# Performance work log

Measured on AMD Instinct MI355X. Metric: run time of the kernel, lower is better.

Reference implementation:

```python
import jax, jax.numpy as jnp
import numpy as np

B, N, D, H = 2, 384, 128, 8

def _ln(x, g, b, eps=1e-5):
    m = jnp.mean(x, -1, keepdims=True)
    v = jnp.mean((x - m) ** 2, -1, keepdims=True)
    return (x - m) * jax.lax.rsqrt(v + eps) * g + b

def _gelu(x):
    return jax.nn.gelu(x, approximate=False)  # torch nn.GELU default = exact erf

def setup_inputs() -> dict:
    key = jax.random.key(0)
    ks = jax.random.split(key, 20)
    def w(i, *s):
        return jax.random.normal(ks[i], s, jnp.float32) * 0.02
    return {
        'node_features': jax.random.normal(ks[0], (B, N, D), jnp.float32),
        'edge_features': jax.random.normal(ks[1], (B, N, N, D), jnp.float32),
        'mask': jnp.ones((B, N), dtype=bool),
        'attn_wqkv_node': w(2, D, 3 * D),
        'attn_wqkv_edge': w(3, D, 4 * D),
        'lin0_w': w(4, D, D), 'lin0_b': jnp.zeros(D, jnp.float32),
        'ln0_g': jnp.ones(D, jnp.float32), 'ln0_bias': jnp.zeros(D, jnp.float32),
        'ln1_g': jnp.ones(D, jnp.float32), 'ln1_bias': jnp.zeros(D, jnp.float32),
        'nmlp_w1': w(5, D, 2 * D), 'nmlp_w2': w(6, 2 * D, D), 'nmlp_b2': jnp.zeros(D, jnp.float32),
        'e0_we': w(7, 2 * D, D), 'e0_be': jnp.zeros(D, jnp.float32),
        'e0_ws': w(8, D, D), 'e0_bs': jnp.zeros(D, jnp.float32),
        'e0_wt': w(9, D, D), 'e0_bt': jnp.zeros(D, jnp.float32),
        'e0_wer': w(10, D, D), 'e0_wec': w(11, D, D),
        'e0_w1': w(12, D, D), 'e0_b1': jnp.zeros(D, jnp.float32),
        'e1_w1': w(13, D, 2 * D), 'e1_w2': w(14, 2 * D, D), 'e1_b2': jnp.zeros(D, jnp.float32),
        'eln0_g': jnp.ones(D, jnp.float32), 'eln0_b': jnp.zeros(D, jnp.float32),
        'eln1_g': jnp.ones(D, jnp.float32), 'eln1_b': jnp.zeros(D, jnp.float32),
    }

def _forward(node, edge, wqkv_n, wqkv_e, lin0_w, lin0_b, ln0_g, ln0_bias, ln1_g, ln1_bias,
             nmlp_w1, nmlp_w2, nmlp_b2, e0_we, e0_be, e0_ws, e0_bs, e0_wt, e0_bt,
             e0_wer, e0_wec, e0_w1, e0_b1, e1_w1, e1_w2, e1_b2, eln0_g, eln0_b, eln1_g, eln1_b):
    b, n, d = node.shape
    h = H
    dh = d // h
    scale = 1.0 / (d ** 0.5)  # note: scale uses full d_hid as in source
    # ---- RTAttention (modulate_v=True) ----
    qkv_n = (node @ wqkv_n).reshape(b, n, h, 3 * dh).transpose(0, 2, 1, 3)  # b h n 3dh
    qn, kn, vn = jnp.split(qkv_n, 3, axis=-1)
    qkv_e = (edge @ wqkv_e).reshape(b, n, n, h, 4 * dh).transpose(0, 3, 1, 2, 4)  # b h i j 4dh
    eq, ek, ev, em = jnp.split(qkv_e, 4, axis=-1)
    q = qn[:, :, :, None, :] + eq                      # b h i j dh
    k = kn[:, :, None, :, :] + ek
    v = vn[:, :, None, :, :] * em + ev                 # modulate_v: v_node*edge[3] + edge[2]
    dots = scale * jnp.einsum('bhijd,bhijd->bhij', q, k)
    attn = jax.nn.softmax(dots, axis=-1)
    out = jnp.einsum('bhij,bhijd->bhid', attn, v)
    out = out.transpose(0, 2, 1, 3).reshape(b, n, d)
    # ---- node updates, type 'rt' (dropout=0 -> identity) ----
    x = _ln(node + (out @ lin0_w + lin0_b), ln0_g, ln0_bias)
    x = _ln(x + (_gelu(x @ nmlp_w1) @ nmlp_w2 + nmlp_b2), ln1_g, ln1_bias)
    # ---- edge updates: EdgeMLP ----
    sn = (x @ e0_ws + e0_bs)[:, :, None, :]                       # broadcast over j
    tn = (x @ e0_wt + e0_bt)[:, None, :, :]                       # broadcast over i
    se = jnp.mean(edge, axis=1, keepdims=True) @ e0_wec           # mean over dim -3, lin0_ec
    te = jnp.mean(edge, axis=2, keepdims=True) @ e0_wer           # mean over dim -2, lin0_er
    e = jnp.concatenate([edge, jnp.swapaxes(edge, 1, 2)], axis=-1) @ e0_we + e0_be
    e = _gelu(e + sn + tn + se + te) @ e0_w1 + e0_b1
    edge2 = _ln(edge + e, eln0_g, eln0_b)
    edge2 = _ln(edge2 + (_gelu(edge2 @ e1_w1) @ e1_w2 + e1_b2), eln1_g, eln1_b)
    return x, edge2

def reference(node_features, edge_features, mask, attn_wqkv_node, attn_wqkv_edge,
              lin0_w, lin0_b, ln0_g, ln0_bias, ln1_g, ln1_bias,
              nmlp_w1, nmlp_w2, nmlp_b2, e0_we, e0_be, e0_ws, e0_bs, e0_wt, e0_bt,
              e0_wer, e0_wec, e0_w1, e0_b1, e1_w1, e1_w2, e1_b2,
              eln0_g, eln0_b, eln1_g, eln1_b):
    # mask is accepted but unused by the source forward path
    return _forward(node_features, edge_features, attn_wqkv_node, attn_wqkv_edge,
                    lin0_w, lin0_b, ln0_g, ln0_bias, ln1_g, ln1_bias,
                    nmlp_w1, nmlp_w2, nmlp_b2, e0_we, e0_be, e0_ws, e0_bs, e0_wt, e0_bt,
                    e0_wer, e0_wec, e0_w1, e0_b1, e1_w1, e1_w2, e1_b2,
                    eln0_g, eln0_b, eln1_g, eln1_b)
```

## Files before the change

### kernel.cpp

```cpp
#include <hip/hip_runtime.h>
#include <hip/hip_bf16.h>
#include <cstdint>
#include <cstddef>

#define B_ 2
#define N_ 384
#define D_ 128
#define NN (N_*N_)
#define BN (B_*N_)
#define EDGE_ELEMS (B_*NN*D_)
#define NODE_ELEMS (BN*D_)

typedef short bh8 __attribute__((ext_vector_type(8)));
typedef float f32x4 __attribute__((ext_vector_type(4)));

__device__ __forceinline__ f32x4 mfma_bf16(bh8 a, bh8 b, f32x4 c){
  return __builtin_amdgcn_mfma_f32_16x16x32_bf16(a, b, c, 0, 0, 0);
}
__device__ __forceinline__ unsigned short f2bf(float f){
  unsigned u = __float_as_uint(f);
  return (unsigned short)((u + 0x7fffu + ((u >> 16) & 1u)) >> 16);
}
__device__ __forceinline__ unsigned f2bf_pk(float a, float b){
  __hip_bfloat162 h = __float22bfloat162_rn(make_float2(a, b));
  return *(unsigned*)&h;
}
__device__ __forceinline__ float bf2f(unsigned short h){
  return __uint_as_float(((unsigned)h) << 16);
}
__device__ __forceinline__ float geluf(float x){
  return 0.5f * x * (1.0f + erff(x * 0.70710678118654752f));
}
__device__ __forceinline__ float gelu_fast(float x){
  float x2 = x * x;
  float t  = __fmaf_rn(0.044715f * x, x2, x);
  float e  = __expf(1.5957691216057308f * t);
  float r  = __builtin_amdgcn_rcpf(e + 1.0f);
  return x - x * r;
}
__device__ __forceinline__ f32x4 zero4(){ f32x4 z = {0.f,0.f,0.f,0.f}; return z; }

__device__ __forceinline__ float red16_add(float x){
  x += __int_as_float(__builtin_amdgcn_update_dpp(0, __float_as_int(x), 0xB1, 0xF, 0xF, true));
  x += __int_as_float(__builtin_amdgcn_update_dpp(0, __float_as_int(x), 0x4E, 0xF, 0xF, true));
  x += __int_as_float(__builtin_amdgcn_update_dpp(0, __float_as_int(x), 0x141, 0xF, 0xF, true));
  x += __int_as_float(__builtin_amdgcn_update_dpp(0, __float_as_int(x), 0x140, 0xF, 0xF, true));
  return x;
}
__device__ __forceinline__ float red4_add(float x){
  x += __int_as_float(__builtin_amdgcn_update_dpp(0, __float_as_int(x), 0xB1, 0xF, 0xF, true));
  x += __int_as_float(__builtin_amdgcn_update_dpp(0, __float_as_int(x), 0x4E, 0xF, 0xF, true));
  return x;
}
__device__ __forceinline__ int swz(int m, int c){
  return ((((c >> 3) ^ (m & 7)) << 3) | (c & 7));
}

__global__ void kprep(const float* wqkv_e, const float* e0_we, const float* e0_w1,
                      const float* e1_w1, const float* e1_w2,
                      const float* node, const float* wqkv_n,
                      unsigned short* WqkvT, unsigned short* WeT, unsigned short* W1T,
                      unsigned short* E1W1T, unsigned short* E1W2T,
                      float* qkvn){
  int m = blockIdx.y;
  int tid = threadIdx.x;
  if (m < 5){
    const float* src; unsigned short* dst; int K, Nn;
    if (m == 0){ src = wqkv_e; dst = WqkvT; K = 128; Nn = 512; }
    else if (m == 1){ src = e0_we; dst = WeT;   K = 256; Nn = 128; }
    else if (m == 2){ src = e0_w1; dst = W1T;   K = 128; Nn = 128; }
    else if (m == 3){ src = e1_w1; dst = E1W1T; K = 128; Nn = 256; }
    else            { src = e1_w2; dst = E1W2T; K = 256; Nn = 128; }
    int idx = blockIdx.x * 384 + tid;
    if (idx < K * Nn){
      int n = idx / K, k = idx % K;
      dst[idx] = f2bf(src[k * Nn + n]);
    }
  } else {
    int row = blockIdx.x;
    __shared__ float sn[128];
    if (tid < 128) sn[tid] = node[row * 128 + tid];
    __syncthreads();
    float acc = 0.f;
    #pragma unroll 8
    for (int k = 0; k < 128; ++k) acc += sn[k] * wqkv_n[k * 384 + tid];
    qkvn[row * 384 + tid] = acc;
  }
}

__global__ void kprepA(const float* __restrict__ edge, unsigned short* __restrict__ E16,
                       float* __restrict__ meanJ){
  __shared__ float red[8][128];
  int bi = blockIdx.x; int tid = threadIdx.x;
  const float4* src = (const float4*)(edge + (size_t)bi * N_ * D_);
  uint2* gdst = (uint2*)E16 + (size_t)bi * (N_ * D_ / 4);
  float ps0 = 0.f, ps1 = 0.f, ps2 = 0.f, ps3 = 0.f;
  #pragma unroll 4
  for (int k = 0; k < 48; ++k){
    int idx = k * 256 + tid;
    float4 v = src[idx];
    uint2 o;
    o.x = f2bf_pk(v.x, v.y);
    o.y = f2bf_pk(v.z, v.w);
    gdst[idx] = o;
    ps0 += v.x; ps1 += v.y; ps2 += v.z; ps3 += v.w;
  }
  int g = tid >> 5, d0 = (tid & 31) * 4;
  red[g][d0] = ps0; red[g][d0 + 1] = ps1; red[g][d0 + 2] = ps2; red[g][d0 + 3] = ps3;
  __syncthreads();
  if (tid < 128){
    float s = 0.f;
    #pragma unroll
    for (int gg = 0; gg < 8; ++gg) s += red[gg][tid];
    meanJ[bi * 128 + tid] = s * (1.0f / N_);
  }
}

__global__ __launch_bounds__(256, 2) void kattnI(
    const unsigned short* __restrict__ E16, const unsigned short* __restrict__ WqkvT,
    const float* __restrict__ qkvn, float* __restrict__ attn,
    float* __restrict__ meanI){
  __shared__ float red[16][128];
  int tid = threadIdx.x;
  if (blockIdx.y == 1){
    int bj = blockIdx.x; int b = bj / N_, j = bj % N_;
    int ig = tid >> 4, dsub = tid & 15;
    float acc[8];
    #pragma unroll
    for (int e = 0; e < 8; ++e) acc[e] = 0.f;
    #pragma unroll 4
    for (int i = ig; i < N_; i += 16){
      const unsigned short* p = E16 + ((size_t)(b * N_ + i) * N_ + j) * D_ + dsub * 8;
      uint4 u = *(const uint4*)p;
      acc[0] += bf2f((unsigned short)(u.x & 0xffff)); acc[1] += bf2f((unsigned short)(u.x >> 16));
      acc[2] += bf2f((unsigned short)(u.y & 0xffff)); acc[3] += bf2f((unsigned short)(u.y >> 16));
      acc[4] += bf2f((unsigned short)(u.z & 0xffff)); acc[5] += bf2f((unsigned short)(u.z >> 16));
      acc[6] += bf2f((unsigned short)(u.w & 0xffff)); acc[7] += bf2f((unsigned short)(u.w >> 16));
    }
    #pragma unroll
    for (int e = 0; e < 8; ++e) red[ig][dsub * 8 + e] = acc[e];
    __syncthreads();
    if (tid < 128){
      float s = 0.f;
      #pragma unroll
      for (int gg = 0; gg < 16; ++gg) s += red[gg][tid];
      meanI[bj * 128 + tid] = s * (1.0f / N_);
    }
    return;
  }
  int bi = blockIdx.x; int b = bi / N_;
  int w = tid >> 6, lane = tid & 63, quad = lane >> 4, c16 = lane & 15;
  const float scale = 0.08838834764831845f;
  const unsigned short* Abase = E16 + (size_t)bi * N_ * D_;

  bh8 bf[2][4][4];
  #pragma unroll
  for (int s = 0; s < 2; ++s){
    int h = w + s * 4;
    #pragma unroll
    for (int u = 0; u < 4; ++u)
      #pragma unroll
      for (int ks = 0; ks < 4; ++ks){
        int col = h * 64 + u * 16 + c16;
        bf[s][u][ks] = *(const bh8*)(WqkvT + col * 128 + ks * 32 + quad * 8);
      }
  }
  float qv[2];
  #pragma unroll
  for (int s = 0; s < 2; ++s) qv[s] = qkvn[bi * 384 + (w + s * 4) * 48 + c16];

  float m_run[2] = {-1e30f, -1e30f}, l_run[2] = {0.f, 0.f}, o[2] = {0.f, 0.f};
  bh8 af[4];
  #pragma unroll
  for (int ks = 0; ks < 4; ++ks)
    af[ks] = *(const bh8*)(Abase + (size_t)c16 * D_ + ks * 32 + quad * 8);

  for (int jt = 0; jt < 24; ++jt){
    int jn = (jt + 1 < 24) ? jt + 1 : 0;
    bh8 afn[4];
    #pragma unroll
    for (int ks = 0; ks < 4; ++ks)
      afn[ks] = *(const bh8*)(Abase + (size_t)(jn * 16 + c16) * D_ + ks * 32 + quad * 8);
    float knv[2][4], vnv[2][4];
    const float* kvb = qkvn + ((size_t)b * N_ + jt * 16 + quad * 4) * 384;
    #pragma unroll
    for (int s = 0; s < 2; ++s)
      #pragma unroll
      for (int r = 0; r < 4; ++r){
        knv[s][r] = kvb[r * 384 + (w + s * 4) * 48 + 16 + c16];
        vnv[s][r] = kvb[r * 384 + (w + s * 4) * 48 + 32 + c16];
      }
    f32x4 EQ[2], EK[2], EV[2], EM[2];
    #pragma unroll
    for (int s = 0; s < 2; ++s){ EQ[s] = zero4(); EK[s] = zero4(); EV[s] = zero4(); EM[s] = zero4(); }
    #pragma unroll
    for (int ks = 0; ks < 4; ++ks)
      #pragma unroll
      for (int s = 0; s < 2; ++s){
        EQ[s] = mfma_bf16(af[ks], bf[s][0][ks], EQ[s]);
        EK[s] = mfma_bf16(af[ks], bf[s][1][ks], EK[s]);
        EV[s] = mfma_bf16(af[ks], bf[s][2][ks], EV[s]);
        EM[s] = mfma_bf16(af[ks], bf[s][3][ks], EM[s]);
      }
    #pragma unroll
    for (int s = 0; s < 2; ++s){
      float dots[4], vv[4];
      #pragma unroll
      for (int r = 0; r < 4; ++r){
        float t1 = (qv[s] + EQ[s][r]) * (knv[s][r] + EK[s][r]);
        dots[r] = red16_add(t1) * scale;
        vv[r] = vnv[s][r] * EM[s][r] + EV[s][r];
      }
      float tmax = fmaxf(fmaxf(dots[0], dots[1]), fmaxf(dots[2], dots[3]));
      tmax = fmaxf(tmax, __shfl_xor(tmax, 16));
      tmax = fmaxf(tmax, __shfl_xor(tmax, 32));
      float mnew = fmaxf(m_run[s], tmax);
      float al = __expf(m_run[s] - mnew);
      float p0 = __expf(dots[0] - mnew), p1 = __expf(dots[1] - mnew);
      float p2 = __expf(dots[2] - mnew), p3 = __expf(dots[3] - mnew);
      float lt = p0 + p1 + p2 + p3;
      lt += __shfl_xor(lt, 16); lt += __shfl_xor(lt, 32);
      l_run[s] = l_run[s] * al + lt;
      m_run[s] = mnew;
      o[s] = o[s] * al + p0 * vv[0] + p1 * vv[1] + p2 * vv[2] + p3 * vv[3];
    }
    #pragma unroll
    for (int ks = 0; ks < 4; ++ks) af[ks] = afn[ks];
  }
  #pragma unroll
  for (int s = 0; s < 2; ++s){
    float oo = o[s];
    oo += __shfl_xor(oo, 16); oo += __shfl_xor(oo, 32);
    oo /= l_run[s];
    if (quad == 0) attn[(size_t)bi * D_ + (w + s * 4) * 16 + c16] = oo;
  }
}

__global__ void knodeadd(const float* __restrict__ node, const float* __restrict__ attn,
                         const float* lin0_w, const float* lin0_b,
                         const float* g0, const float* bb0,
                         const float* w1, const float* w2, const float* b2,
                         const float* g1, const float* bb1,
                         const float* __restrict__ meanJ, const float* __restrict__ meanI,
                         const float* ws, const float* bs, const float* wt, const float* bt,
                         const float* wer, const float* wec, const float* be,
                         float* __restrict__ xOut,
                         float* __restrict__ rowAdd, float* __restrict__ colAdd){
  int row = blockIdx.x; int tid = threadIdx.x;
  __shared__ float sa[128], sx[128], sh[256], rb[8], sx2[128], smJ[128], smI[128];
  if (tid < 128){
    sa[tid] = attn[row * 128 + tid];
    smJ[tid] = meanJ[row * 128 + tid];
    smI[tid] = meanI[row * 128 + tid];
  }
  __syncthreads();
  float y = 0.f, x0 = 0.f;
  if (tid < 128){
    float acc = lin0_b[tid];
    #pragma unroll 8
    for (int k = 0; k < 128; ++k) acc += sa[k] * lin0_w[k * 128 + tid];
    y = acc + node[row * 128 + tid];
  }
  { float sv = (tid < 128) ? y : 0.f, sq = (tid < 128) ? y * y : 0.f;
    sv = red16_add(sv); sq = red16_add(sq);
    sv += __shfl_xor(sv, 16); sq += __shfl_xor(sq, 16);
    sv += __shfl_xor(sv, 32); sq += __shfl_xor(sq, 32);
    if ((tid & 63) == 0){ rb[tid >> 6] = sv; rb[4 + (tid >> 6)] = sq; } }
  __syncthreads();
  float mean = (rb[0] + rb[1] + rb[2] + rb[3]) * (1.f / 128.f);
  float var  = (rb[4] + rb[5] + rb[6] + rb[7]) * (1.f / 128.f) - mean * mean;
  float rstd = rsqrtf(var + 1e-5f);
  if (tid < 128){ x0 = (y - mean) * rstd * g0[tid] + bb0[tid]; sx[tid] = x0; }
  __syncthreads();
  { float acc = 0.f;
    #pragma unroll 8
    for (int k = 0; k < 128; ++k) acc += sx[k] * w1[k * 256 + tid];
    sh[tid] = geluf(acc); }
  __syncthreads();
  float y2 = 0.f;
  if (tid < 128){
    float acc = b2[tid];
    #pragma unroll 8
    for (int e = 0; e < 256; ++e) acc += sh[e] * w2[e * 128 + tid];
    y2 = acc + x0;
  }
  __syncthreads();
  { float sv = (tid < 128) ? y2 : 0.f, sq = (tid < 128) ? y2 * y2 : 0.f;
    sv = red16_add(sv); sq = red16_add(sq);
    sv += __shfl_xor(sv, 16); sq += __shfl_xor(sq, 16);
    sv += __shfl_xor(sv, 32); sq += __shfl_xor(sq, 32);
    if ((tid & 63) == 0){ rb[tid >> 6] = sv; rb[4 + (tid >> 6)] = sq; } }
  __syncthreads();
  mean = (rb[0] + rb[1] + rb[2] + rb[3]) * (1.f / 128.f);
  var  = (rb[4] + rb[5] + rb[6] + rb[7]) * (1.f / 128.f) - mean * mean;
  rstd = rsqrtf(var + 1e-5f);
  if (tid < 128){
    float xv = (y2 - mean) * rstd * g1[tid] + bb1[tid];
    xOut[row * 128 + tid] = xv;
    sx2[tid] = xv;
  }
  __syncthreads();
  if (tid < 128){
    int d = tid;
    float s1 = bs[d], s3 = 0.f;
    #pragma unroll 8
    for (int k = 0; k < 128; ++k){
      s1 += sx2[k] * ws[k * 128 + d];
      s3 += smJ[k] * wer[k * 128 + d];
    }
    rowAdd[row * 128 + d] = s1 + s3 + be[d];
  } else {
    int d = tid - 128;
    float s2 = bt[d], s4 = 0.f;
    #pragma unroll 8
    for (int k = 0; k < 128; ++k){
      s2 += sx2[k] * wt[k * 128 + d];
      s4 += smI[k] * wec[k * 128 + d];
    }
    colAdd[row * 128 + d] = s2 + s4;
  }
}

__global__ __launch_bounds__(256, 3) void kedge4(
    const unsigned short* __restrict__ E16, const unsigned short* __restrict__ WeT,
    const unsigned short* __restrict__ W1T, const unsigned short* __restrict__ E1W1T,
    const unsigned short* __restrict__ E1W2T,
    const float* __restrict__ rowAdd, const float* __restrict__ colAdd,
    const float* __restrict__ b1, const float* __restrict__ eg0, const float* __restrict__ eb0,
    const float* __restrict__ e1b2, const float* __restrict__ eg1, const float* __restrict__ eb1,
    float* __restrict__ eOut){
  __shared__ unsigned short sA[64][256];
  __shared__ unsigned short sT[64][128];
  __shared__ float lrS[4][64], lrQ[4][64];
  __shared__ float2 stats[64];
  int tid = threadIdx.x;
  int w = tid >> 6, lane = tid & 63, quad = lane >> 4, c16 = lane & 15;
  int R0 = blockIdx.x * 64;
  int b = R0 / NN; int rem = R0 % NN; int i = rem / N_; int j0 = rem % N_;

  bh8 wb1[2][8];
  #pragma unroll
  for (int t = 0; t < 2; ++t)
    #pragma unroll
    for (int ks = 0; ks < 8; ++ks){
      int col = w * 32 + t * 16 + c16;
      wb1[t][ks] = *(const bh8*)(WeT + (size_t)col * 256 + ks * 32 + quad * 8);
    }
  float ca[2][16], rAv[2];
  #pragma unroll
  for (int t = 0; t < 2; ++t){
    rAv[t] = rowAdd[(b * N_ + i) * D_ + w * 32 + t * 16 + c16];
    #pragma unroll
    for (int ms = 0; ms < 4; ++ms)
      #pragma unroll
      for (int r = 0; r < 4; ++r)
        ca[t][ms * 4 + r] = colAdd[(size_t)(b * N_ + j0 + ms * 16 + quad * 4 + r) * D_
                                   + w * 32 + t * 16 + c16];
  }

  #pragma unroll
  for (int it = 0; it < 8; ++it){
    int cid = it * 256 + tid;
    int rrow = cid >> 5;
    int chunk = cid & 31;
    int kc = chunk * 8;
    const unsigned short* sp;
    if (kc < 128) sp = E16 + ((size_t)(b * N_ + i) * N_ + (j0 + rrow)) * D_ + kc;
    else          sp = E16 + ((size_t)(b * N_ + j0 + rrow) * N_ + i) * D_ + (kc - 128);
    *(float4*)&sA[rrow][(chunk ^ (rrow & 7)) << 3] = *(const float4*)sp;
  }
  __syncthreads();

  f32x4 acc1[2][4];
  #pragma unroll
  for (int t = 0; t < 2; ++t) for (int ms = 0; ms < 4; ++ms) acc1[t][ms] = zero4();
  #pragma unroll
  for (int ks = 0; ks < 8; ++ks){
    bh8 af[4];
    #pragma unroll
    for (int ms = 0; ms < 4; ++ms)
      af[ms] = *(const bh8*)&sA[ms * 16 + c16][((ks * 4 + quad) ^ (c16 & 7)) << 3];
    #pragma unroll
    for (int t = 0; t < 2; ++t)
      #pragma unroll
      for (int ms = 0; ms < 4; ++ms)
        acc1[t][ms] = mfma_bf16(af[ms], wb1[t][ks], acc1[t][ms]);
  }
  #pragma unroll
  for (int ms = 0; ms < 4; ++ms)
    #pragma unroll
    for (int r = 0; r < 4; ++r){
      int m = ms * 16 + quad * 4 + r;
      float v0 = gelu_fast(acc1[0][ms][r] + rAv[0] + ca[0][ms * 4 + r]);
      float v1 = gelu_fast(acc1[1][ms][r] + rAv[1] + ca[1][ms * 4 + r]);
      unsigned pk = f2bf_pk(v0, v1);
      sT[m][swz(m, w * 32 + c16)]      = (unsigned short)(pk & 0xffff);
      sT[m][swz(m, w * 32 + 16 + c16)] = (unsigned short)(pk >> 16);
    }
  __syncthreads();

  bh8 wb2[2][4];
  #pragma unroll
  for (int t = 0; t < 2; ++t)
    #pragma unroll
    for (int ks = 0; ks < 4; ++ks){
      int col = w * 32 + t * 16 + c16;
      wb2[t][ks] = *(const bh8*)(W1T + (size_t)col * 128 + ks * 32 + quad * 8);
    }
  f32x4 acc2[2][4];
  #pragma unroll
  for (int t = 0; t < 2; ++t) for (int ms = 0; ms < 4; ++ms) acc2[t][ms] = zero4();
  #pragma unroll
  for (int ks = 0; ks < 4; ++ks){
    bh8 af[4];
    #pragma unroll
    for (int ms = 0; ms < 4; ++ms)
      af[ms] = *(const bh8*)&sT[ms * 16 + c16][((ks * 4 + quad) ^ (c16 & 7)) << 3];
    #pragma unroll
    for (int t = 0; t < 2; ++t)
      #pragma unroll
      for (int ms = 0; ms < 4; ++ms)
        acc2[t][ms] = mfma_bf16(af[ms], wb2[t][ks], acc2[t][ms]);
  }
  float b1v[2], g0v[2], b0v[2];
  #pragma unroll
  for (int t = 0; t < 2; ++t){
    int c = w * 32 + t * 16 + c16;
    b1v[t] = b1[c]; g0v[t] = eg0[c]; b0v[t] = eb0[c];
  }
  #pragma unroll
  for (int ms = 0; ms < 4; ++ms)
    #pragma unroll
    for (int r = 0; r < 4; ++r){
      int m = ms * 16 + quad * 4 + r;
      float s = 0.f, q = 0.f;
      #pragma unroll
      for (int t = 0; t < 2; ++t){
        float v = acc2[t][ms][r] + b1v[t] + bf2f(sA[m][swz(m, w * 32 + t * 16 + c16)]);
        acc2[t][ms][r] = v; s += v; q += v * v;
      }
      s = red16_add(s); q = red16_add(q);
      if (c16 == 0){ lrS[w][m] = s; lrQ[w][m] = q; }
    }
  __syncthreads();
  {
    int src = lane & 3, mrow = w * 16 + (lane >> 2);
    float sp = lrS[src][mrow], qp = lrQ[src][mrow];
    sp = red4_add(sp); qp = red4_add(qp);
    if (src == 0){
      float mean = sp * (1.f / 128.f);
      float var  = qp * (1.f / 128.f) - mean * mean;
      stats[mrow] = make_float2(mean, rsqrtf(var + 1e-5f));
    }
  }
  __syncthreads();
  #pragma unroll
  for (int ms = 0; ms < 4; ++ms)
    #pragma unroll
    for (int r = 0; r < 4; ++r){
      int m = ms * 16 + quad * 4 + r;
      float2 st = stats[m];
      float e0 = (acc2[0][ms][r] - st.x) * st.y * g0v[0] + b0v[0];
      float e1 = (acc2[1][ms][r] - st.x) * st.y * g0v[1] + b0v[1];
      unsigned pk = f2bf_pk(e0, e1);
      sA[m][swz(m, w * 32 + c16)]      = (unsigned short)(pk & 0xffff);
      sA[m][swz(m, w * 32 + 16 + c16)] = (unsigned short)(pk >> 16);
    }
  __syncthreads();

  f32x4 acc4[2][4];
  #pragma unroll
  for (int t = 0; t < 2; ++t) for (int ms = 0; ms < 4; ++ms) acc4[t][ms] = zero4();
  #pragma unroll
  for (int p = 0; p < 2; ++p){
    bh8 wb3[2][4];
    #pragma unroll
    for (int t = 0; t < 2; ++t)
      #pragma unroll
      for (int ks = 0; ks < 4; ++ks){
        int col = p * 128 + w * 32 + t * 16 + c16;
        wb3[t][ks] = *(const bh8*)(E1W1T + (size_t)col * 128 + ks * 32 + quad * 8);
      }
    f32x4 acc3[2][4];
    #pragma unroll
    for (int t = 0; t < 2; ++t) for (int ms = 0; ms < 4; ++ms) acc3[t][ms] = zero4();
    #pragma unroll
    for (int ks = 0; ks < 4; ++ks){
      bh8 af[4];
      #pragma unroll
      for (int ms = 0; ms < 4; ++ms)
        af[ms] = *(const bh8*)&sA[ms * 16 + c16][((ks * 4 + quad) ^ (c16 & 7)) << 3];
      #pragma unroll
      for (int t = 0; t < 2; ++t)
        #pragma unroll
        for (int ms = 0; ms < 4; ++ms)
          acc3[t][ms] = mfma_bf16(af[ms], wb3[t][ks], acc3[t][ms]);
    }
    #pragma unroll
    for (int ms = 0; ms < 4; ++ms)
      #pragma unroll
      for (int r = 0; r < 4; ++r){
        int m = ms * 16 + quad * 4 + r;
        float v0 = gelu_fast(acc3[0][ms][r]);
        float v1 = gelu_fast(acc3[1][ms][r]);
        unsigned pk = f2bf_pk(v0, v1);
        sT[m][swz(m, w * 32 + c16)]      = (unsigned short)(pk & 0xffff);
        sT[m][swz(m, w * 32 + 16 + c16)] = (unsigned short)(pk >> 16);
      }
    __syncthreads();
    bh8 wb4[2][4];
    #pragma unroll
    for (int t = 0; t < 2; ++t)
      #pragma unroll
      for (int k2 = 0; k2 < 4; ++k2){
        int col = w * 32 + t * 16 + c16;
        wb4[t][k2] = *(const bh8*)(E1W2T + (size_t)col * 256 + p * 128 + k2 * 32 + quad * 8);
      }
    #pragma unroll
    for (int k2 = 0; k2 < 4; ++k2){
      bh8 af[4];
      #pragma unroll
      for (int ms = 0; ms < 4; ++ms)
        af[ms] = *(const bh8*)&sT[ms * 16 + c16][((k2 * 4 + quad) ^ (c16 & 7)) << 3];
      #pragma unroll
      for (int t = 0; t < 2; ++t)
        #pragma unroll
        for (int ms = 0; ms < 4; ++ms)
          acc4[t][ms] = mfma_bf16(af[ms], wb4[t][k2], acc4[t][ms]);
    }
    __syncthreads();
  }

  float b2v[2], g1v[2], bb1v[2];
  #pragma unroll
  for (int t = 0; t < 2; ++t){
    int c = w * 32 + t * 16 + c16;
    b2v[t] = e1b2[c]; g1v[t] = eg1[c]; bb1v[t] = eb1[c];
  }
  #pragma unroll
  for (int ms = 0; ms < 4; ++ms)
    #pragma unroll
    for (int r = 0; r < 4; ++r){
      int m = ms * 16 + quad * 4 + r;
      float s = 0.f, q = 0.f;
      #pragma unroll
      for (int t = 0; t < 2; ++t){
        float v = acc4[t][ms][r] + b2v[t] + bf2f(sA[m][swz(m, w * 32 + t * 16 + c16)]);
        acc4[t][ms][r] = v; s += v; q += v * v;
      }
      s = red16_add(s); q = red16_add(q);
      if (c16 == 0){ lrS[w][m] = s; lrQ[w][m] = q; }
    }
  __syncthreads();
  {
    int src = lane & 3, mrow = w * 16 + (lane >> 2);
    float sp = lrS[src][mrow], qp = lrQ[src][mrow];
    sp = red4_add(sp); qp = red4_add(qp);
    if (src == 0){
      float mean = sp * (1.f / 128.f);
      float var  = qp * (1.f / 128.f) - mean * mean;
      stats[mrow] = make_float2(mean, rsqrtf(var + 1e-5f));
    }
  }
  __syncthreads();
  float* outBase = eOut + ((size_t)(b * N_ + i) * N_ + j0) * D_;
  #pragma unroll
  for (int ms = 0; ms < 4; ++ms)
    #pragma unroll
    for (int r = 0; r < 4; ++r){
      int m = ms * 16 + quad * 4 + r;
      float2 st = stats[m];
      #pragma unroll
      for (int t = 0; t < 2; ++t){
        int c = w * 32 + t * 16 + c16;
        outBase[(size_t)m * D_ + c] = (acc4[t][ms][r] - st.x) * st.y * g1v[t] + bb1v[t];
      }
    }
}

extern "C" void kernel_launch(void* const* d_in, const int* in_sizes, int n_in,
                              void* d_out, int out_size, void* d_ws, size_t ws_size,
                              hipStream_t stream){
  const float* node   = (const float*)d_in[0];
  const float* edge   = (const float*)d_in[1];
  const float* wqkv_n = (const float*)d_in[3];
  const float* wqkv_e = (const float*)d_in[4];
  const float* lin0_w = (const float*)d_in[5];
  const float* lin0_b = (const float*)d_in[6];
  const float* ln0_g  = (const float*)d_in[7];
  const float* ln0_b  = (const float*)d_in[8];
  const float* ln1_g  = (const float*)d_in[9];
  const float* ln1_b  = (const float*)d_in[10];
  const float* nmlp_w1= (const float*)d_in[11];
  const float* nmlp_w2= (const float*)d_in[12];
  const float* nmlp_b2= (const float*)d_in[13];
  const float* e0_we  = (const float*)d_in[14];
  const float* e0_be  = (const float*)d_in[15];
  const float* e0_ws  = (const float*)d_in[16];
  const float* e0_bs  = (const float*)d_in[17];
  const float* e0_wt  = (const float*)d_in[18];
  const float* e0_bt  = (const float*)d_in[19];
  const float* e0_wer = (const float*)d_in[20];
  const float* e0_wec = (const float*)d_in[21];
  const float* e0_w1  = (const float*)d_in[22];
  const float* e0_b1  = (const float*)d_in[23];
  const float* e1_w1  = (const float*)d_in[24];
  const float* e1_w2  = (const float*)d_in[25];
  const float* e1_b2  = (const float*)d_in[26];
  const float* eln0_g = (const float*)d_in[27];
  const float* eln0_b = (const float*)d_in[28];
  const float* eln1_g = (const float*)d_in[29];
  const float* eln1_b = (const float*)d_in[30];

  unsigned short* E16   = (unsigned short*)d_ws;
  unsigned short* WqkvT = E16 + (size_t)EDGE_ELEMS;
  unsigned short* WeT   = WqkvT + 65536;
  unsigned short* W1T   = WeT + 32768;
  unsigned short* E1W1T = W1T + 16384;
  unsigned short* E1W2T = E1W1T + 32768;
  float* fbase  = (float*)(E1W2T + 32768);
  float* qkvn   = fbase;
  float* attn   = qkvn + (size_t)BN * 384;
  float* meanJ  = attn + NODE_ELEMS;
  float* meanI  = meanJ + NODE_ELEMS;
  float* rowAdd = meanI + NODE_ELEMS;
  float* colAdd = rowAdd + NODE_ELEMS;

  float* xOut = (float*)d_out;
  float* eOut = xOut + NODE_ELEMS;

  kprep<<<dim3(BN, 6), 384, 0, stream>>>(wqkv_e, e0_we, e0_w1, e1_w1, e1_w2,
                                         node, wqkv_n,
                                         WqkvT, WeT, W1T, E1W1T, E1W2T, qkvn);
  kprepA<<<BN, 256, 0, stream>>>(edge, E16, meanJ);
  kattnI<<<dim3(BN, 2), 256, 0, stream>>>(E16, WqkvT, qkvn, attn, meanI);
  knodeadd<<<BN, 256, 0, stream>>>(node, attn, lin0_w, lin0_b, ln0_g, ln0_b,
                                   nmlp_w1, nmlp_w2, nmlp_b2, ln1_g, ln1_b,
                                   meanJ, meanI, e0_ws, e0_bs, e0_wt, e0_bt,
                                   e0_wer, e0_wec, e0_be,
                                   xOut, rowAdd, colAdd);
  kedge4<<<NN * B_ / 64, 256, 0, stream>>>(E16, WeT, W1T, E1W1T, E1W2T,
                                           rowAdd, colAdd, e0_b1,
                                           eln0_g, eln0_b, e1_b2, eln1_g, eln1_b,
                                           eOut);
}
```

Baseline: 636.0 us.

## Reuse sA for intermediates, permute weight K order, raise kedge4 occupancy

Removes the separate sT, reduction and stats shared buffers in kedge4 and stores GELU intermediates and LayerNorm partials in the upper half of sA. The K dimension of the W1/E1W1/E1W2 weights is permuted at prep time, so each lane writes adjacent output columns as one packed 32-bit LDS store and one float2 global store. Launch bounds go from 3 to 5 blocks per CU to use the freed LDS. The rowAdd/colAdd loads move after the first GEMM to shorten register live ranges. The cost is extra barriers and a possible risk of register spills under the tighter bound.

```diff
diff --git a/kernel.cpp b/kernel.cpp
--- a/kernel.cpp
+++ b/kernel.cpp
@@ -52,8 +52,11 @@
   x += __int_as_float(__builtin_amdgcn_update_dpp(0, __float_as_int(x), 0x4E, 0xF, 0xF, true));
   return x;
 }
-__device__ __forceinline__ int swz(int m, int c){
-  return ((((c >> 3) ^ (m & 7)) << 3) | (c & 7));
+__device__ __forceinline__ int swz(int m, int p){
+  return ((((p >> 3) ^ (m & 7)) << 3) | (p & 7));
+}
+__device__ __forceinline__ int PHIDX(int x){
+  return (x & ~31) | ((x & 1) << 4) | ((x & 31) >> 1);
 }
 
 __global__ void kprep(const float* wqkv_e, const float* e0_we, const float* e0_w1,
@@ -74,7 +77,8 @@
     int idx = blockIdx.x * 384 + tid;
     if (idx < K * Nn){
       int n = idx / K, k = idx % K;
-      dst[idx] = f2bf(src[k * Nn + n]);
+      int ksrc = (m >= 2) ? ((k & ~127) | PHIDX(k & 127)) : k;
+      dst[idx] = f2bf(src[ksrc * Nn + n]);
     }
   } else {
     int row = blockIdx.x;
@@ -321,7 +325,7 @@
   }
 }
 
-__global__ __launch_bounds__(256, 3) void kedge4(
+__global__ __launch_bounds__(256, 5) void kedge4(
     const unsigned short* __restrict__ E16, const unsigned short* __restrict__ WeT,
     const unsigned short* __restrict__ W1T, const unsigned short* __restrict__ E1W1T,
     const unsigned short* __restrict__ E1W2T,
@@ -330,9 +334,7 @@
     const float* __restrict__ e1b2, const float* __restrict__ eg1, const float* __restrict__ eb1,
     float* __restrict__ eOut){
   __shared__ unsigned short sA[64][256];
-  __shared__ unsigned short sT[64][128];
-  __shared__ float lrS[4][64], lrQ[4][64];
-  __shared__ float2 stats[64];
+#define HIFV(i) (((float*)&sA[0][0])[ (((i) >> 6) << 7) + 64 + ((i) & 63) ])
   int tid = threadIdx.x;
   int w = tid >> 6, lane = tid & 63, quad = lane >> 4, c16 = lane & 15;
   int R0 = blockIdx.x * 64;
@@ -346,17 +348,6 @@
       int col = w * 32 + t * 16 + c16;
       wb1[t][ks] = *(const bh8*)(WeT + (size_t)col * 256 + ks * 32 + quad * 8);
     }
-  float ca[2][16], rAv[2];
-  #pragma unroll
-  for (int t = 0; t < 2; ++t){
-    rAv[t] = rowAdd[(b * N_ + i) * D_ + w * 32 + t * 16 + c16];
-    #pragma unroll
-    for (int ms = 0; ms < 4; ++ms)
-      #pragma unroll
-      for (int r = 0; r < 4; ++r)
-        ca[t][ms * 4 + r] = colAdd[(size_t)(b * N_ + j0 + ms * 16 + quad * 4 + r) * D_
-                                   + w * 32 + t * 16 + c16];
-  }
 
   #pragma unroll
   for (int it = 0; it < 8; ++it){
@@ -378,14 +369,29 @@
   for (int ks = 0; ks < 8; ++ks){
     bh8 af[4];
     #pragma unroll
-    for (int ms = 0; ms < 4; ++ms)
-      af[ms] = *(const bh8*)&sA[ms * 16 + c16][((ks * 4 + quad) ^ (c16 & 7)) << 3];
+    for (int ms = 0; ms < 4; ++ms){
+      int row = ms * 16 + c16;
+      af[ms] = *(const bh8*)&sA[row][swz(row, ks * 32 + quad * 8)];
+    }
     #pragma unroll
     for (int t = 0; t < 2; ++t)
       #pragma unroll
       for (int ms = 0; ms < 4; ++ms)
         acc1[t][ms] = mfma_bf16(af[ms], wb1[t][ks], acc1[t][ms]);
   }
+  float rAv[2], ca[2][16];
+  #pragma unroll
+  for (int t = 0; t < 2; ++t){
+    rAv[t] = rowAdd[(b * N_ + i) * D_ + w * 32 + t * 16 + c16];
+    #pragma unroll
+    for (int ms = 0; ms < 4; ++ms)
+      #pragma unroll
+      for (int r = 0; r < 4; ++r)
+        ca[t][ms * 4 + r] = colAdd[(size_t)(b * N_ + j0 + ms * 16 + quad * 4 + r) * D_
+                                   + w * 32 + t * 16 + c16];
+  }
+  __syncthreads();
+
   #pragma unroll
   for (int ms = 0; ms < 4; ++ms)
     #pragma unroll
@@ -393,9 +399,7 @@
       int m = ms * 16 + quad * 4 + r;
       float v0 = gelu_fast(acc1[0][ms][r] + rAv[0] + ca[0][ms * 4 + r]);
       float v1 = gelu_fast(acc1[1][ms][r] + rAv[1] + ca[1][ms * 4 + r]);
-      unsigned pk = f2bf_pk(v0, v1);
-      sT[m][swz(m, w * 32 + c16)]      = (unsigned short)(pk & 0xffff);
-      sT[m][swz(m, w * 32 + 16 + c16)] = (unsigned short)(pk >> 16);
+      *(unsigned*)&sA[m][swz(m, 128 + w * 32 + c16 * 2)] = f2bf_pk(v0, v1);
     }
   __syncthreads();
 
@@ -414,8 +418,10 @@
   for (int ks = 0; ks < 4; ++ks){
     bh8 af[4];
     #pragma unroll
-    for (int ms = 0; ms < 4; ++ms)
-      af[ms] = *(const bh8*)&sT[ms * 16 + c16][((ks * 4 + quad) ^ (c16 & 7)) << 3];
+    for (int ms = 0; ms < 4; ++ms){
+      int row = ms * 16 + c16;
+      af[ms] = *(const bh8*)&sA[row][swz(row, 128 + ks * 32 + quad * 8)];
+    }
     #pragma unroll
     for (int t = 0; t < 2; ++t)
       #pragma unroll
@@ -428,6 +434,7 @@
     int c = w * 32 + t * 16 + c16;
     b1v[t] = b1[c]; g0v[t] = eg0[c]; b0v[t] = eb0[c];
   }
+  __syncthreads();
   #pragma unroll
   for (int ms = 0; ms < 4; ++ms)
     #pragma unroll
@@ -440,17 +447,18 @@
         acc2[t][ms][r] = v; s += v; q += v * v;
       }
       s = red16_add(s); q = red16_add(q);
-      if (c16 == 0){ lrS[w][m] = s; lrQ[w][m] = q; }
+      if (c16 == 0){ HIFV(w * 64 + m) = s; HIFV(256 + w * 64 + m) = q; }
     }
   __syncthreads();
   {
     int src = lane & 3, mrow = w * 16 + (lane >> 2);
-    float sp = lrS[src][mrow], qp = lrQ[src][mrow];
+    float sp = HIFV(src * 64 + mrow), qp = HIFV(256 + src * 64 + mrow);
     sp = red4_add(sp); qp = red4_add(qp);
     if (src == 0){
       float mean = sp * (1.f / 128.f);
       float var  = qp * (1.f / 128.f) - mean * mean;
-      stats[mrow] = make_float2(mean, rsqrtf(var + 1e-5f));
+      HIFV(512 + 2 * mrow) = mean;
+      HIFV(513 + 2 * mrow) = rsqrtf(var + 1e-5f);
     }
   }
   __syncthreads();
@@ -459,12 +467,10 @@
     #pragma unroll
     for (int r = 0; r < 4; ++r){
       int m = ms * 16 + quad * 4 + r;
-      float2 st = stats[m];
+      float2 st = *(float2*)&HIFV(512 + 2 * m);
       float e0 = (acc2[0][ms][r] - st.x) * st.y * g0v[0] + b0v[0];
       float e1 = (acc2[1][ms][r] - st.x) * st.y * g0v[1] + b0v[1];
-      unsigned pk = f2bf_pk(e0, e1);
-      sA[m][swz(m, w * 32 + c16)]      = (unsigned short)(pk & 0xffff);
-      sA[m][swz(m, w * 32 + 16 + c16)] = (unsigned short)(pk >> 16);
+      *(unsigned*)&sA[m][swz(m, w * 32 + c16 * 2)] = f2bf_pk(e0, e1);
     }
   __syncthreads();
 
@@ -488,8 +494,10 @@
     for (int ks = 0; ks < 4; ++ks){
       bh8 af[4];
       #pragma unroll
-      for (int ms = 0; ms < 4; ++ms)
-        af[ms] = *(const bh8*)&sA[ms * 16 + c16][((ks * 4 + quad) ^ (c16 & 7)) << 3];
+      for (int ms = 0; ms < 4; ++ms){
+        int row = ms * 16 + c16;
+        af[ms] = *(const bh8*)&sA[row][swz(row, ks * 32 + quad * 8)];
+      }
       #pragma unroll
       for (int t = 0; t < 2; ++t)
         #pragma unroll
@@ -503,9 +511,7 @@
         int m = ms * 16 + quad * 4 + r;
         float v0 = gelu_fast(acc3[0][ms][r]);
         float v1 = gelu_fast(acc3[1][ms][r]);
-        unsigned pk = f2bf_pk(v0, v1);
-        sT[m][swz(m, w * 32 + c16)]      = (unsigned short)(pk & 0xffff);
-        sT[m][swz(m, w * 32 + 16 + c16)] = (unsigned short)(pk >> 16);
+        *(unsigned*)&sA[m][swz(m, 128 + w * 32 + c16 * 2)] = f2bf_pk(v0, v1);
       }
     __syncthreads();
     bh8 wb4[2][4];
@@ -513,15 +519,17 @@
     for (int t = 0; t < 2; ++t)
       #pragma unroll
       for (int k2 = 0; k2 < 4; ++k2){
-        int col = w * 32 + t * 16 + c16;
-        wb4[t][k2] = *(const bh8*)(E1W2T + (size_t)col * 256 + p * 128 + k2 * 32 + quad * 8);
+        int pcol = w * 32 + c16 * 2 + t;
+        wb4[t][k2] = *(const bh8*)(E1W2T + (size_t)pcol * 256 + p * 128 + k2 * 32 + quad * 8);
       }
     #pragma unroll
     for (int k2 = 0; k2 < 4; ++k2){
       bh8 af[4];
       #pragma unroll
-      for (int ms = 0; ms < 4; ++ms)
-        af[ms] = *(const bh8*)&sT[ms * 16 + c16][((k2 * 4 + quad) ^ (c16 & 7)) << 3];
+      for (int ms = 0; ms < 4; ++ms){
+        int row = ms * 16 + c16;
+        af[ms] = *(const bh8*)&sA[row][swz(row, 128 + k2 * 32 + quad * 8)];
+      }
       #pragma unroll
       for (int t = 0; t < 2; ++t)
         #pragma unroll
@@ -531,11 +539,13 @@
     __syncthreads();
   }
 
-  float b2v[2], g1v[2], bb1v[2];
+  float b2v[2], g1v[2], bb1v[2]; int slv[2];
   #pragma unroll
   for (int t = 0; t < 2; ++t){
-    int c = w * 32 + t * 16 + c16;
-    b2v[t] = e1b2[c]; g1v[t] = eg1[c]; bb1v[t] = eb1[c];
+    int pcol = w * 32 + c16 * 2 + t;
+    b2v[t] = e1b2[pcol]; g1v[t] = eg1[pcol]; bb1v[t] = eb1[pcol];
+    int lo5 = c16 * 2 + t;
+    slv[t] = w * 32 + (((lo5 & 15) << 1) | (lo5 >> 4));
   }
   #pragma unroll
   for (int ms = 0; ms < 4; ++ms)
@@ -545,21 +555,22 @@
       float s = 0.f, q = 0.f;
       #pragma unroll
       for (int t = 0; t < 2; ++t){
-        float v = acc4[t][ms][r] + b2v[t] + bf2f(sA[m][swz(m, w * 32 + t * 16 + c16)]);
+        float v = acc4[t][ms][r] + b2v[t] + bf2f(sA[m][swz(m, slv[t])]);
         acc4[t][ms][r] = v; s += v; q += v * v;
       }
       s = red16_add(s); q = red16_add(q);
-      if (c16 == 0){ lrS[w][m] = s; lrQ[w][m] = q; }
+      if (c16 == 0){ HIFV(w * 64 + m) = s; HIFV(256 + w * 64 + m) = q; }
     }
   __syncthreads();
   {
     int src = lane & 3, mrow = w * 16 + (lane >> 2);
-    float sp = lrS[src][mrow], qp = lrQ[src][mrow];
+    float sp = HIFV(src * 64 + mrow), qp = HIFV(256 + src * 64 + mrow);
     sp = red4_add(sp); qp = red4_add(qp);
     if (src == 0){
       float mean = sp * (1.f / 128.f);
       float var  = qp * (1.f / 128.f) - mean * mean;
-      stats[mrow] = make_float2(mean, rsqrtf(var + 1e-5f));
+      HIFV(512 + 2 * mrow) = mean;
+      HIFV(513 + 2 * mrow) = rsqrtf(var + 1e-5f);
     }
   }
   __syncthreads();
@@ -569,13 +580,13 @@
     #pragma unroll
     for (int r = 0; r < 4; ++r){
       int m = ms * 16 + quad * 4 + r;
-      float2 st = stats[m];
-      #pragma unroll
-      for (int t = 0; t < 2; ++t){
-        int c = w * 32 + t * 16 + c16;
-        outBase[(size_t)m * D_ + c] = (acc4[t][ms][r] - st.x) * st.y * g1v[t] + bb1v[t];
-      }
-    }
+      float2 st = *(float2*)&HIFV(512 + 2 * m);
+      float2 ov;
+      ov.x = (acc4[0][ms][r] - st.x) * st.y * g1v[0] + bb1v[0];
+      ov.y = (acc4[1][ms][r] - st.x) * st.y * g1v[1] + bb1v[1];
+      *(float2*)&outBase[(size_t)m * D_ + w * 32 + c16 * 2] = ov;
+    }
+#undef HIFV
 }
 
 extern "C" void kernel_launch(void* const* d_in, const int* in_sizes, int n_in,
```

Result: slower. 802.2 us (+26.1%).
